# Kernel optimization log

Hardware: AMD Instinct MI355X
Metric: run time of the kernel (lower is better)

## Reference

```python
import jax, jax.numpy as jnp
import numpy as np

B = 4            # number of scenes (equal-size segments; offset = [M,2M,3M,4M])
K_NEAR = 16
K_FAR = 32
K_SMOOTH = 8
T_LOC = 0.1
T_CON = 0.5
BN_EPS = 1e-5


def setup_inputs() -> dict:
    key = jax.random.key(0)
    ks = jax.random.split(key, 8)
    N, C, H, O = 32768, 6, 64, 1
    coords = jax.random.uniform(ks[0], (N, 3), jnp.float32) * 2.0 - 1.0
    feat = jax.random.normal(ks[1], (N, C), jnp.float32)
    return {
        'feat': feat,
        'coords': coords,
        'W1': jax.random.normal(ks[2], (C, H), jnp.float32) * 0.1,
        'b1': jnp.zeros((H,), jnp.float32),
        'g1': jnp.ones((H,), jnp.float32),
        'be1': jnp.zeros((H,), jnp.float32),
        'W2': jax.random.normal(ks[3], (H, H), jnp.float32) * 0.1,
        'b2': jnp.zeros((H,), jnp.float32),
        'g2': jnp.ones((H,), jnp.float32),
        'be2': jnp.zeros((H,), jnp.float32),
        'W3': jax.random.normal(ks[4], (H, O), jnp.float32) * 0.1,
        'b3': jnp.zeros((O,), jnp.float32),
    }


def _bn_train(x, g, b):
    # BatchNorm1d in train mode: biased batch statistics
    mu = x.mean(axis=0)
    var = x.var(axis=0)
    return g * (x - mu) * jax.lax.rsqrt(var + BN_EPS) + b


def _knn_per_scene(c):
    # c: [M,3] -> [M,K_FAR] sorted nearest-neighbor indices (self first)
    sq = jnp.sum(c * c, axis=-1)                       # [M]
    d2 = sq[:, None] + sq[None, :] - 2.0 * (c @ c.T)   # [M,M] GEMM-based
    return jax.lax.top_k(-d2, K_FAR)[1]                # [M,K_FAR]


def _forward(feat, coords, W1, b1, g1, be1, W2, b2, g2, be2, W3, b3):
    N = feat.shape[0]
    M = N // B
    # ---- PointSorter MLP -> ordering scores in (0,1) ----
    h = jax.nn.gelu(_bn_train(feat @ W1 + b1, g1, be1), approximate=False)
    h = jax.nn.gelu(_bn_train(h @ W2 + b2, g2, be2), approximate=False)
    scores = jax.nn.sigmoid(h @ W3 + b3)               # [N, num_orders]
    s = scores.mean(axis=1, keepdims=True)             # [N,1] (scores_mean)
    # ---- single fused KNN (k=32); slice for k=16 (near) and k=8 (smooth) ----
    cb = coords.reshape(B, M, 3)
    idx = jax.vmap(_knn_per_scene)(cb)                 # [B,M,K_FAR] local
    idx = (idx + (jnp.arange(B) * M)[:, None, None]).reshape(N, K_FAR)
    idx_near = idx[:, :K_NEAR]
    idx_far = idx[:, K_NEAR:]
    idx_sm = idx[:, :K_SMOOTH]
    # ---- locality: neighbors should have similar scores ----
    sd = jnp.abs(s[:, None, :] - s[idx_near])[..., 0]          # [N,16]
    diff = coords[:, None, :] - coords[idx_near]               # [N,16,3]
    d = jnp.sqrt(jnp.maximum(jnp.sum(diff * diff, axis=2), 1e-24))
    w = jnp.exp(-d / T_LOC)
    loss_loc = jnp.sum(w * sd * sd) / jnp.maximum(jnp.sum(w), 1e-8)
    # ---- contrastive: far points should have different scores ----
    sim_pos = 1.0 - jnp.abs(s[:, None, :] - s[idx_near])       # [N,16,1]
    sim_neg = 1.0 - jnp.abs(s[:, None, :] - s[idx_far])        # [N,16,1]
    loss_pos = -jnp.mean(jnp.log(jax.nn.sigmoid(sim_pos / T_CON) + 1e-8))
    loss_neg = -jnp.mean(jnp.log(1.0 - jax.nn.sigmoid(sim_neg / T_CON) + 1e-8))
    loss_con = loss_pos + loss_neg
    # ---- smoothness: score close to mean of 8-NN scores ----
    nmean = s[idx_sm].mean(axis=1)                             # [N,1]
    loss_sm = jnp.mean((s - nmean) ** 2)
    return 1.0 * loss_loc + 0.5 * loss_con + 0.2 * loss_sm


def reference(feat, coords, W1, b1, g1, be1, W2, b2, g2, be2, W3, b3):
    return _forward(feat, coords, W1, b1, g1, be1, W2, b2, g2, be2, W3, b3)
```

## Files before the change

### kernel.cpp

```cpp
#include <hip/hip_runtime.h>

typedef unsigned long long u64;
typedef unsigned int u32;
typedef unsigned short u16;

#define N_PTS 32768
#define M_PTS 8192
#define C_IN 6
#define H_DIM 64

#define G 6
#define NCELL 216
#define NCELL_T 864
#define CW (1.0f/3.0f)

#define NBLK 256
#define QG 4
#define KTGT 48.0f

#define TL0 0.0494f
#define TL1 0.0740f
#define TL2 0.1110f
#define TL3 0.1736f
#define TL4 0.2600f
#define TL5 0.4000f


__device__ __forceinline__ float gelu_exact(float x) {
    return 0.5f * x * (1.0f + erff(x * 0.70710678118654752f));
}
__device__ __forceinline__ float sigmoidf_(float x) {
    return 1.0f / (1.0f + expf(-x));
}
__device__ __forceinline__ u64 u64min_(u64 a, u64 b) { return a < b ? a : b; }
__device__ __forceinline__ u64 u64max_(u64 a, u64 b) { return a < b ? b : a; }

__device__ __forceinline__ u64 bitonic_sort64(u64 key, int lane) {
    #pragma unroll
    for (int k = 2; k <= 64; k <<= 1) {
        #pragma unroll
        for (int j = k >> 1; j; j >>= 1) {
            u64 pk = __shfl_xor(key, j, 64);
            bool up = ((lane & k) == 0);
            bool tmin = (((lane & j) == 0) == up);
            key = tmin ? u64min_(key, pk) : u64max_(key, pk);
        }
    }
    return key;
}

__global__ __launch_bounds__(256) void kA(const float* __restrict__ feat,
        const float* __restrict__ coords, const float* __restrict__ W1,
        const float* __restrict__ b1, u32* __restrict__ gcount,
        u16* __restrict__ pcell, float* __restrict__ stats1) {
    __shared__ float red[512];
    int t = threadIdx.x, bid = blockIdx.x;
    if (bid < 128) {
        int n = bid * 256 + t;
        float x = coords[n*3], y = coords[n*3+1], z = coords[n*3+2];
        int cx = min(G-1, max(0, (int)floorf((x + 1.0f) * 3.0f)));
        int cy = min(G-1, max(0, (int)floorf((y + 1.0f) * 3.0f)));
        int cz = min(G-1, max(0, (int)floorf((z + 1.0f) * 3.0f)));
        int gcid = (n >> 13) * NCELL + (cz*G + cy)*G + cx;
        pcell[n] = (u16)gcid;
        atomicAdd(&gcount[gcid], 1u);
    }
    int c = t & 63, w = t >> 6;
    float w1c[C_IN];
    #pragma unroll
    for (int k = 0; k < C_IN; ++k) w1c[k] = W1[k*H_DIM + c];
    float bias = b1[c];
    float s1 = 0.f, s2 = 0.f;
    #pragma unroll 1
    for (int n = bid*8 + w*2; n < N_PTS; n += NBLK*8) {
        const float* fa = feat + n*C_IN;
        const float* fb = feat + (n+1)*C_IN;
        float ha = bias, hb = bias;
        #pragma unroll
        for (int k = 0; k < C_IN; ++k) {
            ha = fmaf(fa[k], w1c[k], ha);
            hb = fmaf(fb[k], w1c[k], hb);
        }
        s1 += ha + hb;
        s2 = fmaf(ha, ha, s2); s2 = fmaf(hb, hb, s2);
    }
    red[w*64 + c] = s1;
    red[256 + w*64 + c] = s2;
    __syncthreads();
    if (t < 64) {
        float a = red[t] + red[64+t] + red[128+t] + red[192+t];
        float b = red[256+t] + red[320+t] + red[384+t] + red[448+t];
        atomicAdd(&stats1[t], a);
        atomicAdd(&stats1[64+t], b);
    }
}

__global__ __launch_bounds__(256) void kB(const float* __restrict__ feat,
        const float* __restrict__ W1, const float* __restrict__ b1,
        const float* __restrict__ stats1, const float* __restrict__ g1,
        const float* __restrict__ be1, const float* __restrict__ W2,
        const float* __restrict__ b2, const u32* __restrict__ gcount,
        u32* __restrict__ cellstart, u32* __restrict__ cellptr,
        float* __restrict__ stats2) {
    __shared__ float red[512];
    __shared__ u32 sc[256];
    int t = threadIdx.x, bid = blockIdx.x;
    if (bid == 0) {
        u32 loc[4]; u32 s = 0;
        #pragma unroll
        for (int j = 0; j < 4; ++j) {
            int idx = t*4 + j;
            loc[j] = (idx < NCELL_T) ? gcount[idx] : 0u;
            s += loc[j];
        }
        sc[t] = s;
        __syncthreads();
        for (int off = 1; off < 256; off <<= 1) {
            u32 v = sc[t];
            if (t >= off) v += sc[t-off];
            __syncthreads();
            sc[t] = v;
            __syncthreads();
        }
        u32 run = sc[t] - s;
        #pragma unroll
        for (int j = 0; j < 4; ++j) {
            int idx = t*4 + j;
            if (idx < NCELL_T) { cellstart[idx] = run; cellptr[idx] = run; }
            run += loc[j];
        }
        if (t == 255) cellstart[NCELL_T] = sc[255];
        __syncthreads();
    }
    int c = t & 63, w = t >> 6;
    float w2c[H_DIM];
    #pragma unroll
    for (int k = 0; k < H_DIM; ++k) w2c[k] = W2[k*H_DIM + c];
    float w1c[C_IN];
    #pragma unroll
    for (int k = 0; k < C_IN; ++k) w1c[k] = W1[k*H_DIM + c];
    float mean1 = stats1[c] * (1.0f/N_PTS);
    float var1  = stats1[64+c] * (1.0f/N_PTS) - mean1*mean1;
    float sc1 = g1[c] * rsqrtf(var1 + 1e-5f);
    float sh1 = be1[c] - mean1*sc1;
    float bias1 = b1[c], bias2 = b2[c];
    float s1 = 0.f, s2 = 0.f;
    #pragma unroll 1
    for (int n = bid*8 + w*2; n < N_PTS; n += NBLK*8) {
        const float* fa = feat + n*C_IN;
        const float* fb = feat + (n+1)*C_IN;
        float ha = bias1, hb = bias1;
        #pragma unroll
        for (int k = 0; k < C_IN; ++k) {
            ha = fmaf(fa[k], w1c[k], ha);
            hb = fmaf(fb[k], w1c[k], hb);
        }
        float aa = gelu_exact(fmaf(sc1, ha, sh1));
        float ab = gelu_exact(fmaf(sc1, hb, sh1));
        float h2a = bias2, h2b = bias2;
        #pragma unroll
        for (int k = 0; k < H_DIM; ++k) {
            h2a = fmaf(__shfl(aa, k, 64), w2c[k], h2a);
            h2b = fmaf(__shfl(ab, k, 64), w2c[k], h2b);
        }
        s1 += h2a + h2b;
        s2 = fmaf(h2a, h2a, s2); s2 = fmaf(h2b, h2b, s2);
    }
    red[w*64 + c] = s1;
    red[256 + w*64 + c] = s2;
    __syncthreads();
    if (t < 64) {
        float a = red[t] + red[64+t] + red[128+t] + red[192+t];
        float b = red[256+t] + red[320+t] + red[384+t] + red[448+t];
        atomicAdd(&stats2[t], a);
        atomicAdd(&stats2[64+t], b);
    }
}

__global__ __launch_bounds__(256) void kC(const float* __restrict__ feat,
        const float* __restrict__ coords,
        const float* __restrict__ W1, const float* __restrict__ b1,
        const float* __restrict__ stats1, const float* __restrict__ g1,
        const float* __restrict__ be1, const float* __restrict__ W2,
        const float* __restrict__ b2, const float* __restrict__ stats2,
        const float* __restrict__ g2v, const float* __restrict__ be2,
        const float* __restrict__ W3, const float* __restrict__ b3,
        const u16* __restrict__ pcell, u32* __restrict__ cellptr,
        float4* __restrict__ P4s, u16* __restrict__ meta16,
        float* __restrict__ S) {
    int t = threadIdx.x, bid = blockIdx.x;
    if (bid < 128) {
        int n = bid * 256 + t;
        float x = coords[n*3], y = coords[n*3+1], z = coords[n*3+2];
        float sq = fmaf(x, x, fmaf(y, y, z*z));
        u32 pos = atomicAdd(&cellptr[pcell[n]], 1u);
        P4s[pos] = make_float4(x, y, z, sq);
        meta16[pos] = (u16)(n & (M_PTS-1));
    }
    int c = t & 63, w = t >> 6;
    float w2c[H_DIM];
    #pragma unroll
    for (int k = 0; k < H_DIM; ++k) w2c[k] = W2[k*H_DIM + c];
    float w1c[C_IN];
    #pragma unroll
    for (int k = 0; k < C_IN; ++k) w1c[k] = W1[k*H_DIM + c];
    float mean1 = stats1[c] * (1.0f/N_PTS);
    float var1  = stats1[64+c] * (1.0f/N_PTS) - mean1*mean1;
    float sc1 = g1[c] * rsqrtf(var1 + 1e-5f);
    float sh1 = be1[c] - mean1*sc1;
    float mean2 = stats2[c] * (1.0f/N_PTS);
    float var2  = stats2[64+c] * (1.0f/N_PTS) - mean2*mean2;
    float sc2 = g2v[c] * rsqrtf(var2 + 1e-5f);
    float sh2 = be2[c] - mean2*sc2;
    float bias1 = b1[c], bias2 = b2[c], w3 = W3[c], bb = b3[0];
    #pragma unroll 1
    for (int n = bid*8 + w*2; n < N_PTS; n += NBLK*8) {
        const float* fa = feat + n*C_IN;
        const float* fb = feat + (n+1)*C_IN;
        float ha = bias1, hb = bias1;
        #pragma unroll
        for (int k = 0; k < C_IN; ++k) {
            ha = fmaf(fa[k], w1c[k], ha);
            hb = fmaf(fb[k], w1c[k], hb);
        }
        float aa = gelu_exact(fmaf(sc1, ha, sh1));
        float ab = gelu_exact(fmaf(sc1, hb, sh1));
        float h2a = bias2, h2b = bias2;
        #pragma unroll
        for (int k = 0; k < H_DIM; ++k) {
            h2a = fmaf(__shfl(aa, k, 64), w2c[k], h2a);
            h2b = fmaf(__shfl(ab, k, 64), w2c[k], h2b);
        }
        float a2a = gelu_exact(fmaf(sc2, h2a, sh2));
        float a2b = gelu_exact(fmaf(sc2, h2b, sh2));
        float va = a2a * w3, vb = a2b * w3;
        #pragma unroll
        for (int m = 32; m; m >>= 1) {
            va += __shfl_xor(va, m, 64);
            vb += __shfl_xor(vb, m, 64);
        }
        if (c == 0) {
            S[n] = sigmoidf_(va + bb);
            S[n+1] = sigmoidf_(vb + bb);
        }
    }
}

__global__ __launch_bounds__(256) void kD(const float4* __restrict__ P4s,
        const u16* __restrict__ meta16, const u32* __restrict__ cellstart,
        const float* __restrict__ S, double* __restrict__ accum,
        u32* __restrict__ donecnt, float* __restrict__ out) {
    __shared__ u64 wavebuf[4][QG][128];
    __shared__ int runsb[16], runse[16];
    __shared__ int nruns_s;
    __shared__ u32 flistB[64];
    __shared__ u32 flnB;
    __shared__ u32 cnt6[6];
    __shared__ u32 ovcnt;
    __shared__ float smacc;
    __shared__ double lred[4][5];

    int t = threadIdx.x, bid = blockIdx.x;
    int lane = t & 63, w = t >> 6;
    u64 lmask = (1ull << lane) - 1ull;
    int cell = bid >> 1, half = bid & 1;
    int scene = cell / NCELL;
    int cid = cell - scene*NCELL;
    int cx = cid % G, cy = (cid / G) % G, cz = cid / (G*G);
    int sbase = scene * M_PTS;

    int ccrd[3] = {cx, cy, cz};
    bool wall[3]; int Wn = 0;
    #pragma unroll
    for (int d = 0; d < 3; ++d) { wall[d] = (ccrd[d] == 0 || ccrd[d] == G-1); Wn += wall[d]; }
    int lo[3], hi[3];
    #pragma unroll
    for (int d = 0; d < 3; ++d) {
        if (Wn >= 2 && !wall[d]) { lo[d] = min(max(ccrd[d]-2, 0), G-5); hi[d] = lo[d]+4; }
        else                     { lo[d] = min(max(ccrd[d]-1, 0), G-3); hi[d] = lo[d]+2; }
    }
    float lof[3], hif[3]; bool lw[3], hw[3];
    #pragma unroll
    for (int d = 0; d < 3; ++d) {
        lof[d] = -1.0f + lo[d]*CW; hif[d] = -1.0f + (hi[d]+1)*CW;
        lw[d] = (lo[d] == 0); hw[d] = (hi[d] == G-1);
    }
    if (t == 0) {
        int nr = 0;
        int nx = hi[0]-lo[0]+1;
        for (int z = lo[2]; z <= hi[2]; ++z)
            for (int y = lo[1]; y <= hi[1]; ++y) {
                int bc = scene*NCELL + (z*G + y)*G + lo[0];
                runsb[nr] = (int)cellstart[bc];
                runse[nr] = (int)cellstart[bc + nx];
                ++nr;
            }
        nruns_s = nr;
        flnB = 0;
    }
    int gcid = scene*NCELL + cid;
    int qstart = (int)cellstart[gcid];
    int qn = (int)cellstart[gcid+1] - qstart;
    __syncthreads();
    int nruns = nruns_s;
    int hq = (qn + 1) >> 1;
    int hqs = qstart + half * hq;
    int hqn = qn - half * hq; if (hqn > hq) hqn = hq; if (hqn < 0) hqn = 0;

    double anum=0.0, aden=0.0, aslp=0.0, asln=0.0, asmo=0.0;

    for (int g0 = w*QG; g0 < hqn; g0 += 4*QG) {
        int jcount = min(QG, hqn - g0);
        int qb = hqs + g0;
        float qx[QG], qy[QG], qz[QG], qs[QG], tp[QG];
        u32 baseq[QG];
        #pragma unroll
        for (int j = 0; j < QG; ++j) {
            int qg = qb + min(j, jcount-1);
            float4 qc = P4s[qg];
            qx[j]=qc.x; qy[j]=qc.y; qz[j]=qc.z; qs[j]=qc.w;
            float cov = 1e9f;
            float qdv[3] = {qc.x, qc.y, qc.z};
            #pragma unroll
            for (int d = 0; d < 3; ++d) {
                if (!lw[d]) cov = fminf(cov, qdv[d] - lof[d]);
                if (!hw[d]) cov = fminf(cov, hif[d] - qdv[d]);
            }
            float g2 = cov*cov;
            float axx = fminf(qc.x+1.f, 1.f-qc.x);
            float ayy = fminf(qc.y+1.f, 1.f-qc.y);
            float azz = fminf(qc.z+1.f, 1.f-qc.z);
            float r = 0.224f;
            #pragma unroll
            for (int it = 0; it < 3; ++it) {
                float ir = 1.0f / r;
                float ux = fminf(axx*ir, 1.f), uy = fminf(ayy*ir, 1.f), uz = fminf(azz*ir, 1.f);
                float fx = 0.25f*(2.f + 3.f*ux - ux*ux*ux);
                float fy = 0.25f*(2.f + 3.f*uy - uy*uy*uy);
                float fz = 0.25f*(2.f + 3.f*uz - uz*uz*uz);
                r = cbrtf(KTGT / (4289.32f * fx * fy * fz));
            }
            tp[j] = (j < jcount) ? (fminf(r*r, g2) - qc.w) : -1e30f;
            baseq[j] = 0;
        }

        for (int rr = 0; rr < nruns; ++rr) {
            int ve = runse[rr];
            for (int v0 = runsb[rr]; v0 < ve; v0 += 128) {
                int vA = v0 + lane, vB = v0 + 64 + lane;
                bool okA = vA < ve, okB = vB < ve;
                float4 pA = make_float4(0.f,0.f,0.f,1e30f);
                float4 pB = make_float4(0.f,0.f,0.f,1e30f);
                u32 mA = 0, mB = 0;
                if (okA) { pA = P4s[vA]; mA = (u32)meta16[vA]; }
                if (okB) { pB = P4s[vB]; mB = (u32)meta16[vB]; }
                #pragma unroll
                for (int j = 0; j < QG; ++j) {
                    float dotA = fmaf(qx[j], pA.x, fmaf(qy[j], pA.y, qz[j]*pA.z));
                    float e2A = fmaf(-2.0f, dotA, pA.w);
                    bool prA = okA && (e2A < tp[j]);
                    u64 mkA = __ballot(prA);
                    if (prA) {
                        float d2 = fmaxf(e2A + qs[j], 0.0f);
                        u64 key = ((u64)__float_as_uint(d2) << 13) | (u64)mA;
                        u32 pos = baseq[j] + (u32)__popcll(mkA & lmask);
                        if (pos < 128u) wavebuf[w][j][pos] = key;
                    }
                    baseq[j] += (u32)__popcll(mkA);
                    float dotB = fmaf(qx[j], pB.x, fmaf(qy[j], pB.y, qz[j]*pB.z));
                    float e2B = fmaf(-2.0f, dotB, pB.w);
                    bool prB = okB && (e2B < tp[j]);
                    u64 mkB = __ballot(prB);
                    if (prB) {
                        float d2 = fmaxf(e2B + qs[j], 0.0f);
                        u64 key = ((u64)__float_as_uint(d2) << 13) | (u64)mB;
                        u32 pos = baseq[j] + (u32)__popcll(mkB & lmask);
                        if (pos < 128u) wavebuf[w][j][pos] = key;
                    }
                    baseq[j] += (u32)__popcll(mkB);
                }
            }
        }

        #pragma unroll
        for (int j = 0; j < QG; ++j) {
            if (j >= jcount) continue;
            int qg = qb + j;
            u32 M = baseq[j];
            if (M < 32u || M > 128u) {
                if (lane == 0) {
                    u32 idx = atomicAdd(&flnB, 1u);
                    if (idx < 64u) flistB[idx] = (u32)qg;
                }
                continue;
            }
            u64 k0 = (lane < (int)min(M, 64u)) ? wavebuf[w][j][lane] : ~0ull;
            k0 = bitonic_sort64(k0, lane);
            if (M > 64u) {
                u64 k1 = (lane < (int)(M - 64u)) ? wavebuf[w][j][64 + lane] : ~0ull;
                k1 = bitonic_sort64(k1, lane);
                u64 pk = __shfl(k1, 63 - lane, 64);
                u64 lo2 = u64min_(k0, pk);
                #pragma unroll
                for (int jj = 32; jj; jj >>= 1) {
                    u64 pj = __shfl_xor(lo2, jj, 64);
                    lo2 = ((lane & jj) == 0) ? u64min_(lo2, pj) : u64max_(lo2, pj);
                }
                k0 = lo2;
            }
            float si = S[sbase + (int)meta16[qg]];
            float smsum = 0.f;
            if (lane < 32) {
                float d2 = __uint_as_float((u32)(k0 >> 13));
                u32 jo = (u32)(k0 & 0x1FFFu);
                float sj = S[sbase + (int)jo];
                float sd = fabsf(si - sj);
                float sim = 1.0f - sd;
                if (lane < 16) {
                    float d = sqrtf(fmaxf(d2, 1e-24f));
                    float wgt = expf(-10.0f*d);
                    anum += (double)(wgt*sd*sd);
                    aden += (double)wgt;
                    aslp += (double)logf(sigmoidf_(2.0f*sim) + 1e-8f);
                    if (lane < 8) smsum += sj;
                } else {
                    asln += (double)logf(sigmoidf_(-2.0f*sim) + 1e-8f);
                }
            }
            #pragma unroll
            for (int m = 32; m; m >>= 1) smsum += __shfl_xor(smsum, m, 64);
            if (lane == 0) {
                float dd = si - smsum*0.125f;
                asmo += (double)(dd*dd);
            }
        }
    }
    __syncthreads();

    int nf = min((int)flnB, 64);
    u64* ovbuf = &wavebuf[0][0][0];
    for (int f = 0; f < nf; ++f) {
        int fqg = (int)flistB[f];
        float4 fqc = P4s[fqg];
        float fsq = fqc.w;
        float fcov = 1e9f;
        float fqd[3] = {fqc.x, fqc.y, fqc.z};
        #pragma unroll
        for (int d = 0; d < 3; ++d) {
            if (!lw[d]) fcov = fminf(fcov, fqd[d] - lof[d]);
            if (!hw[d]) fcov = fminf(fcov, hif[d] - fqd[d]);
        }
        float fg2 = fcov*fcov;
        if (t < 6) cnt6[t] = 0;
        if (t == 0) { ovcnt = 0; smacc = 0.f; }
        __syncthreads();
        u32 c0=0,c1=0,c2=0,c3=0,c4=0,c5=0;
        for (int rr = 0; rr < nruns; ++rr) {
            for (int v = runsb[rr] + t; v < runse[rr]; v += 256) {
                float4 pp = P4s[v];
                float dot = fmaf(fqc.x, pp.x, fmaf(fqc.y, pp.y, fqc.z*pp.z));
                float e2 = fmaf(-2.0f, dot, pp.w);
                c0 += (e2 < TL0-fsq); c1 += (e2 < TL1-fsq); c2 += (e2 < TL2-fsq);
                c3 += (e2 < TL3-fsq); c4 += (e2 < TL4-fsq); c5 += (e2 < TL5-fsq);
            }
        }
        #pragma unroll
        for (int m = 32; m; m >>= 1) {
            c0 += __shfl_xor(c0, m, 64); c1 += __shfl_xor(c1, m, 64);
            c2 += __shfl_xor(c2, m, 64); c3 += __shfl_xor(c3, m, 64);
            c4 += __shfl_xor(c4, m, 64); c5 += __shfl_xor(c5, m, 64);
        }
        if (lane == 0) {
            atomicAdd(&cnt6[0], c0); atomicAdd(&cnt6[1], c1);
            atomicAdd(&cnt6[2], c2); atomicAdd(&cnt6[3], c3);
            atomicAdd(&cnt6[4], c4); atomicAdd(&cnt6[5], c5);
        }
        __syncthreads();
        float tau = TL2;
        if (TL3 <= fg2) tau = TL3;
        if (TL4 <= fg2) tau = TL4;
        if (TL5 <= fg2) tau = TL5;
        if      (cnt6[0] >= 32u) tau = TL0;
        else if (cnt6[1] >= 32u) tau = TL1;
        else if (cnt6[2] >= 32u) tau = TL2;
        else if (TL3 <= fg2 && cnt6[3] >= 32u) tau = TL3;
        else if (TL4 <= fg2 && cnt6[4] >= 32u) tau = TL4;
        else if (TL5 <= fg2 && cnt6[5] >= 32u) tau = TL5;
        float ftp = tau - fsq;
        for (int rr = 0; rr < nruns; ++rr) {
            for (int v = runsb[rr] + t; v < runse[rr]; v += 256) {
                float4 pp = P4s[v];
                float dot = fmaf(fqc.x, pp.x, fmaf(fqc.y, pp.y, fqc.z*pp.z));
                float e2 = fmaf(-2.0f, dot, pp.w);
                if (e2 < ftp) {
                    float d2 = fmaxf(e2 + fsq, 0.0f);
                    u64 key = ((u64)__float_as_uint(d2) << 13) | (u64)meta16[v];
                    u32 pos = atomicAdd(&ovcnt, 1u);
                    if (pos < 512u) ovbuf[pos] = key;
                }
            }
        }
        __syncthreads();
        u32 Mf = min(ovcnt, 512u);
        float fsi = S[sbase + (int)meta16[fqg]];
        for (int i = t; i < (int)Mf; i += 256) {
            u64 mykey = ovbuf[i];
            u32 rank = 0;
            for (u32 jj = 0; jj < Mf; ++jj) rank += (ovbuf[jj] < mykey);
            if (rank < 32u) {
                float d2 = __uint_as_float((u32)(mykey >> 13));
                u32 jo = (u32)(mykey & 0x1FFFu);
                float sj = S[sbase + (int)jo];
                float sd = fabsf(fsi - sj);
                float sim = 1.0f - sd;
                if (rank < 16u) {
                    float d = sqrtf(fmaxf(d2, 1e-24f));
                    float wgt = expf(-10.0f*d);
                    anum += (double)(wgt*sd*sd);
                    aden += (double)wgt;
                    aslp += (double)logf(sigmoidf_(2.0f*sim) + 1e-8f);
                    if (rank < 8u) atomicAdd(&smacc, sj);
                } else {
                    asln += (double)logf(sigmoidf_(-2.0f*sim) + 1e-8f);
                }
            }
        }
        __syncthreads();
        if (t == 0) {
            float dd = fsi - smacc*0.125f;
            asmo += (double)(dd*dd);
        }
        __syncthreads();
    }

    double v[5] = {anum, aden, aslp, asln, asmo};
    #pragma unroll
    for (int k = 0; k < 5; ++k) {
        for (int m = 32; m; m >>= 1) v[k] += __shfl_xor(v[k], m, 64);
    }
    if (lane == 0) {
        #pragma unroll
        for (int k = 0; k < 5; ++k) lred[w][k] = v[k];
    }
    __syncthreads();
    if (t == 0) {
        #pragma unroll
        for (int k = 0; k < 5; ++k)
            atomicAdd(&accum[k], lred[0][k] + lred[1][k] + lred[2][k] + lred[3][k]);
        __threadfence();
        u32 old = atomicAdd(donecnt, 1u);
        if (old == (u32)(2*NCELL_T - 1)) {
            double a0 = atomicAdd(&accum[0], 0.0);
            double a1 = atomicAdd(&accum[1], 0.0);
            double a2 = atomicAdd(&accum[2], 0.0);
            double a3 = atomicAdd(&accum[3], 0.0);
            double a4 = atomicAdd(&accum[4], 0.0);
            double loss_loc = a0 / fmax(a1, 1e-8);
            double inv = 1.0 / ((double)N_PTS * 16.0);
            double loss_con = -(a2 * inv) - (a3 * inv);
            double loss_sm = a4 / (double)N_PTS;
            out[0] = (float)(loss_loc + 0.5*loss_con + 0.2*loss_sm);
        }
    }
}

extern "C" void kernel_launch(void* const* d_in, const int* in_sizes, int n_in,
                              void* d_out, int out_size, void* d_ws, size_t ws_size,
                              hipStream_t stream) {
    const float* feat   = (const float*)d_in[0];
    const float* coords = (const float*)d_in[1];
    const float* W1 = (const float*)d_in[2];
    const float* b1 = (const float*)d_in[3];
    const float* g1 = (const float*)d_in[4];
    const float* be1= (const float*)d_in[5];
    const float* W2 = (const float*)d_in[6];
    const float* b2 = (const float*)d_in[7];
    const float* g2 = (const float*)d_in[8];
    const float* be2= (const float*)d_in[9];
    const float* W3 = (const float*)d_in[10];
    const float* b3 = (const float*)d_in[11];
    char* ws = (char*)d_ws;

    float* stats1   = (float*)(ws);
    float* stats2   = (float*)(ws + 512);
    u32* gcount     = (u32*)(ws + 1024);
    double* accum   = (double*)(ws + 4480);
    u32* donecnt    = (u32*)(ws + 4520);
    u32* cellstart  = (u32*)(ws + 4544);
    u32* cellptr    = (u32*)(ws + 8008);
    float* S        = (float*)(ws + 11472);
    float4* P4s     = (float4*)(ws + 142544);
    u16* meta16     = (u16*)(ws + 666832);
    u16* pcell      = (u16*)(ws + 732368);

    hipMemsetAsync(d_ws, 0, 4544, stream);

    hipLaunchKernelGGL(kA, dim3(NBLK), dim3(256), 0, stream,
                       feat, coords, W1, b1, gcount, pcell, stats1);
    hipLaunchKernelGGL(kB, dim3(NBLK), dim3(256), 0, stream,
                       feat, W1, b1, stats1, g1, be1, W2, b2,
                       gcount, cellstart, cellptr, stats2);
    hipLaunchKernelGGL(kC, dim3(NBLK), dim3(256), 0, stream,
                       feat, coords, W1, b1, stats1, g1, be1, W2, b2,
                       stats2, g2, be2, W3, b3, pcell, cellptr, P4s, meta16, S);
    hipLaunchKernelGGL(kD, dim3(2*NCELL_T), dim3(256), 0, stream,
                       P4s, meta16, cellstart, S, accum, donecnt, (float*)d_out);
}
```

Baseline: 325.6 us.

## Pack KNN keys into 32 bits, embed index in float4, split cells three ways

KNN sort keys shrink from 64-bit to 32-bit by truncating the distance's low 13 mantissa bits and packing the 13-bit point index there. The local index now lives in the float4 w slot and squared norms are recomputed, which drops the separate meta16 array. Query cells are split across 3 blocks instead of 2, with a retuned neighbor-count target and radius and a larger overflow buffer. The MLP loops now process 4 points per iteration instead of 2. Truncated keys can reorder near-tied neighbors, which may change results slightly.

```diff
diff --git a/kernel.cpp b/kernel.cpp
--- a/kernel.cpp
+++ b/kernel.cpp
@@ -16,7 +16,8 @@
 
 #define NBLK 256
 #define QG 4
-#define KTGT 48.0f
+#define BPC 3
+#define KTGT 54.0f
 
 #define TL0 0.0494f
 #define TL1 0.0740f
@@ -25,6 +26,9 @@
 #define TL4 0.2600f
 #define TL5 0.4000f
 
+#define KEYMASK 0xFFFFE000u
+#define IDXMASK 0x1FFFu
+
 
 __device__ __forceinline__ float gelu_exact(float x) {
     return 0.5f * x * (1.0f + erff(x * 0.70710678118654752f));
@@ -32,18 +36,16 @@
 __device__ __forceinline__ float sigmoidf_(float x) {
     return 1.0f / (1.0f + expf(-x));
 }
-__device__ __forceinline__ u64 u64min_(u64 a, u64 b) { return a < b ? a : b; }
-__device__ __forceinline__ u64 u64max_(u64 a, u64 b) { return a < b ? b : a; }
-
-__device__ __forceinline__ u64 bitonic_sort64(u64 key, int lane) {
+
+__device__ __forceinline__ u32 bitonic_sort64_u32(u32 key, int lane) {
     #pragma unroll
     for (int k = 2; k <= 64; k <<= 1) {
         #pragma unroll
         for (int j = k >> 1; j; j >>= 1) {
-            u64 pk = __shfl_xor(key, j, 64);
+            u32 pk = (u32)__shfl_xor((int)key, j, 64);
             bool up = ((lane & k) == 0);
             bool tmin = (((lane & j) == 0) == up);
-            key = tmin ? u64min_(key, pk) : u64max_(key, pk);
+            key = tmin ? min(key, pk) : max(key, pk);
         }
     }
     return key;
@@ -146,25 +148,28 @@
     float bias1 = b1[c], bias2 = b2[c];
     float s1 = 0.f, s2 = 0.f;
     #pragma unroll 1
-    for (int n = bid*8 + w*2; n < N_PTS; n += NBLK*8) {
-        const float* fa = feat + n*C_IN;
-        const float* fb = feat + (n+1)*C_IN;
-        float ha = bias1, hb = bias1;
-        #pragma unroll
-        for (int k = 0; k < C_IN; ++k) {
-            ha = fmaf(fa[k], w1c[k], ha);
-            hb = fmaf(fb[k], w1c[k], hb);
-        }
-        float aa = gelu_exact(fmaf(sc1, ha, sh1));
-        float ab = gelu_exact(fmaf(sc1, hb, sh1));
-        float h2a = bias2, h2b = bias2;
+    for (int n = bid*16 + w*4; n < N_PTS; n += NBLK*16) {
+        float h[4], a[4], h2[4];
+        #pragma unroll
+        for (int p = 0; p < 4; ++p) {
+            const float* f = feat + (n+p)*C_IN;
+            h[p] = bias1;
+            #pragma unroll
+            for (int k = 0; k < C_IN; ++k) h[p] = fmaf(f[k], w1c[k], h[p]);
+            a[p] = gelu_exact(fmaf(sc1, h[p], sh1));
+            h2[p] = bias2;
+        }
         #pragma unroll
         for (int k = 0; k < H_DIM; ++k) {
-            h2a = fmaf(__shfl(aa, k, 64), w2c[k], h2a);
-            h2b = fmaf(__shfl(ab, k, 64), w2c[k], h2b);
-        }
-        s1 += h2a + h2b;
-        s2 = fmaf(h2a, h2a, s2); s2 = fmaf(h2b, h2b, s2);
+            #pragma unroll
+            for (int p = 0; p < 4; ++p)
+                h2[p] = fmaf(__shfl(a[p], k, 64), w2c[k], h2[p]);
+        }
+        #pragma unroll
+        for (int p = 0; p < 4; ++p) {
+            s1 += h2[p];
+            s2 = fmaf(h2[p], h2[p], s2);
+        }
     }
     red[w*64 + c] = s1;
     red[256 + w*64 + c] = s2;
@@ -186,16 +191,13 @@
         const float* __restrict__ g2v, const float* __restrict__ be2,
         const float* __restrict__ W3, const float* __restrict__ b3,
         const u16* __restrict__ pcell, u32* __restrict__ cellptr,
-        float4* __restrict__ P4s, u16* __restrict__ meta16,
-        float* __restrict__ S) {
+        float4* __restrict__ P4s, float* __restrict__ S) {
     int t = threadIdx.x, bid = blockIdx.x;
     if (bid < 128) {
         int n = bid * 256 + t;
         float x = coords[n*3], y = coords[n*3+1], z = coords[n*3+2];
-        float sq = fmaf(x, x, fmaf(y, y, z*z));
         u32 pos = atomicAdd(&cellptr[pcell[n]], 1u);
-        P4s[pos] = make_float4(x, y, z, sq);
-        meta16[pos] = (u16)(n & (M_PTS-1));
+        P4s[pos] = make_float4(x, y, z, __uint_as_float((u32)(n & (M_PTS-1))));
     }
     int c = t & 63, w = t >> 6;
     float w2c[H_DIM];
@@ -214,43 +216,44 @@
     float sh2 = be2[c] - mean2*sc2;
     float bias1 = b1[c], bias2 = b2[c], w3 = W3[c], bb = b3[0];
     #pragma unroll 1
-    for (int n = bid*8 + w*2; n < N_PTS; n += NBLK*8) {
-        const float* fa = feat + n*C_IN;
-        const float* fb = feat + (n+1)*C_IN;
-        float ha = bias1, hb = bias1;
-        #pragma unroll
-        for (int k = 0; k < C_IN; ++k) {
-            ha = fmaf(fa[k], w1c[k], ha);
-            hb = fmaf(fb[k], w1c[k], hb);
-        }
-        float aa = gelu_exact(fmaf(sc1, ha, sh1));
-        float ab = gelu_exact(fmaf(sc1, hb, sh1));
-        float h2a = bias2, h2b = bias2;
+    for (int n = bid*16 + w*4; n < N_PTS; n += NBLK*16) {
+        float h[4], a[4], h2[4];
+        #pragma unroll
+        for (int p = 0; p < 4; ++p) {
+            const float* f = feat + (n+p)*C_IN;
+            h[p] = bias1;
+            #pragma unroll
+            for (int k = 0; k < C_IN; ++k) h[p] = fmaf(f[k], w1c[k], h[p]);
+            a[p] = gelu_exact(fmaf(sc1, h[p], sh1));
+            h2[p] = bias2;
+        }
         #pragma unroll
         for (int k = 0; k < H_DIM; ++k) {
-            h2a = fmaf(__shfl(aa, k, 64), w2c[k], h2a);
-            h2b = fmaf(__shfl(ab, k, 64), w2c[k], h2b);
-        }
-        float a2a = gelu_exact(fmaf(sc2, h2a, sh2));
-        float a2b = gelu_exact(fmaf(sc2, h2b, sh2));
-        float va = a2a * w3, vb = a2b * w3;
+            #pragma unroll
+            for (int p = 0; p < 4; ++p)
+                h2[p] = fmaf(__shfl(a[p], k, 64), w2c[k], h2[p]);
+        }
+        float v[4];
+        #pragma unroll
+        for (int p = 0; p < 4; ++p)
+            v[p] = gelu_exact(fmaf(sc2, h2[p], sh2)) * w3;
         #pragma unroll
         for (int m = 32; m; m >>= 1) {
-            va += __shfl_xor(va, m, 64);
-            vb += __shfl_xor(vb, m, 64);
+            #pragma unroll
+            for (int p = 0; p < 4; ++p) v[p] += __shfl_xor(v[p], m, 64);
         }
         if (c == 0) {
-            S[n] = sigmoidf_(va + bb);
-            S[n+1] = sigmoidf_(vb + bb);
+            #pragma unroll
+            for (int p = 0; p < 4; ++p) S[n+p] = sigmoidf_(v[p] + bb);
         }
     }
 }
 
 __global__ __launch_bounds__(256) void kD(const float4* __restrict__ P4s,
-        const u16* __restrict__ meta16, const u32* __restrict__ cellstart,
-        const float* __restrict__ S, double* __restrict__ accum,
-        u32* __restrict__ donecnt, float* __restrict__ out) {
-    __shared__ u64 wavebuf[4][QG][128];
+        const u32* __restrict__ cellstart, const float* __restrict__ S,
+        double* __restrict__ accum, u32* __restrict__ donecnt,
+        float* __restrict__ out) {
+    __shared__ u32 wavebuf[4][QG][128];
     __shared__ int runsb[16], runse[16];
     __shared__ int nruns_s;
     __shared__ u32 flistB[64];
@@ -263,7 +266,7 @@
     int t = threadIdx.x, bid = blockIdx.x;
     int lane = t & 63, w = t >> 6;
     u64 lmask = (1ull << lane) - 1ull;
-    int cell = bid >> 1, half = bid & 1;
+    int cell = bid / BPC, part = bid - cell*BPC;
     int scene = cell / NCELL;
     int cid = cell - scene*NCELL;
     int cx = cid % G, cy = (cid / G) % G, cz = cid / (G*G);
@@ -303,9 +306,9 @@
     int qn = (int)cellstart[gcid+1] - qstart;
     __syncthreads();
     int nruns = nruns_s;
-    int hq = (qn + 1) >> 1;
-    int hqs = qstart + half * hq;
-    int hqn = qn - half * hq; if (hqn > hq) hqn = hq; if (hqn < 0) hqn = 0;
+    int hq = (qn + BPC - 1) / BPC;
+    int hqs = qstart + part * hq;
+    int hqn = qn - part * hq; if (hqn > hq) hqn = hq; if (hqn < 0) hqn = 0;
 
     double anum=0.0, aden=0.0, aslp=0.0, asln=0.0, asmo=0.0;
 
@@ -313,12 +316,15 @@
         int jcount = min(QG, hqn - g0);
         int qb = hqs + g0;
         float qx[QG], qy[QG], qz[QG], qs[QG], tp[QG];
-        u32 baseq[QG];
+        u32 qid[QG], baseq[QG];
         #pragma unroll
         for (int j = 0; j < QG; ++j) {
             int qg = qb + min(j, jcount-1);
             float4 qc = P4s[qg];
-            qx[j]=qc.x; qy[j]=qc.y; qz[j]=qc.z; qs[j]=qc.w;
+            qx[j]=qc.x; qy[j]=qc.y; qz[j]=qc.z;
+            qid[j] = __float_as_uint(qc.w);
+            float qsq = fmaf(qc.x, qc.x, fmaf(qc.y, qc.y, qc.z*qc.z));
+            qs[j] = qsq;
             float cov = 1e9f;
             float qdv[3] = {qc.x, qc.y, qc.z};
             #pragma unroll
@@ -330,7 +336,7 @@
             float axx = fminf(qc.x+1.f, 1.f-qc.x);
             float ayy = fminf(qc.y+1.f, 1.f-qc.y);
             float azz = fminf(qc.z+1.f, 1.f-qc.z);
-            float r = 0.224f;
+            float r = 0.233f;
             #pragma unroll
             for (int it = 0; it < 3; ++it) {
                 float ir = 1.0f / r;
@@ -340,7 +346,7 @@
                 float fz = 0.25f*(2.f + 3.f*uz - uz*uz*uz);
                 r = cbrtf(KTGT / (4289.32f * fx * fy * fz));
             }
-            tp[j] = (j < jcount) ? (fminf(r*r, g2) - qc.w) : -1e30f;
+            tp[j] = (j < jcount) ? (fminf(r*r, g2) - qsq) : -1e30f;
             baseq[j] = 0;
         }
 
@@ -349,31 +355,32 @@
             for (int v0 = runsb[rr]; v0 < ve; v0 += 128) {
                 int vA = v0 + lane, vB = v0 + 64 + lane;
                 bool okA = vA < ve, okB = vB < ve;
-                float4 pA = make_float4(0.f,0.f,0.f,1e30f);
-                float4 pB = make_float4(0.f,0.f,0.f,1e30f);
-                u32 mA = 0, mB = 0;
-                if (okA) { pA = P4s[vA]; mA = (u32)meta16[vA]; }
-                if (okB) { pB = P4s[vB]; mB = (u32)meta16[vB]; }
+                float4 pA = make_float4(1e3f,1e3f,1e3f,0.f);
+                float4 pB = make_float4(1e3f,1e3f,1e3f,0.f);
+                if (okA) pA = P4s[vA];
+                if (okB) pB = P4s[vB];
+                float sqA = fmaf(pA.x, pA.x, fmaf(pA.y, pA.y, pA.z*pA.z));
+                float sqB = fmaf(pB.x, pB.x, fmaf(pB.y, pB.y, pB.z*pB.z));
                 #pragma unroll
                 for (int j = 0; j < QG; ++j) {
                     float dotA = fmaf(qx[j], pA.x, fmaf(qy[j], pA.y, qz[j]*pA.z));
-                    float e2A = fmaf(-2.0f, dotA, pA.w);
+                    float e2A = fmaf(-2.0f, dotA, sqA);
                     bool prA = okA && (e2A < tp[j]);
                     u64 mkA = __ballot(prA);
                     if (prA) {
                         float d2 = fmaxf(e2A + qs[j], 0.0f);
-                        u64 key = ((u64)__float_as_uint(d2) << 13) | (u64)mA;
+                        u32 key = (__float_as_uint(d2) & KEYMASK) | __float_as_uint(pA.w);
                         u32 pos = baseq[j] + (u32)__popcll(mkA & lmask);
                         if (pos < 128u) wavebuf[w][j][pos] = key;
                     }
                     baseq[j] += (u32)__popcll(mkA);
                     float dotB = fmaf(qx[j], pB.x, fmaf(qy[j], pB.y, qz[j]*pB.z));
-                    float e2B = fmaf(-2.0f, dotB, pB.w);
+                    float e2B = fmaf(-2.0f, dotB, sqB);
                     bool prB = okB && (e2B < tp[j]);
                     u64 mkB = __ballot(prB);
                     if (prB) {
                         float d2 = fmaxf(e2B + qs[j], 0.0f);
-                        u64 key = ((u64)__float_as_uint(d2) << 13) | (u64)mB;
+                        u32 key = (__float_as_uint(d2) & KEYMASK) | __float_as_uint(pB.w);
                         u32 pos = baseq[j] + (u32)__popcll(mkB & lmask);
                         if (pos < 128u) wavebuf[w][j][pos] = key;
                     }
@@ -394,25 +401,25 @@
                 }
                 continue;
             }
-            u64 k0 = (lane < (int)min(M, 64u)) ? wavebuf[w][j][lane] : ~0ull;
-            k0 = bitonic_sort64(k0, lane);
+            u32 k0 = (lane < (int)min(M, 64u)) ? wavebuf[w][j][lane] : 0xFFFFFFFFu;
+            k0 = bitonic_sort64_u32(k0, lane);
             if (M > 64u) {
-                u64 k1 = (lane < (int)(M - 64u)) ? wavebuf[w][j][64 + lane] : ~0ull;
-                k1 = bitonic_sort64(k1, lane);
-                u64 pk = __shfl(k1, 63 - lane, 64);
-                u64 lo2 = u64min_(k0, pk);
+                u32 k1 = (lane < (int)(M - 64u)) ? wavebuf[w][j][64 + lane] : 0xFFFFFFFFu;
+                k1 = bitonic_sort64_u32(k1, lane);
+                u32 pk = (u32)__shfl((int)k1, 63 - lane, 64);
+                u32 lo2 = min(k0, pk);
                 #pragma unroll
                 for (int jj = 32; jj; jj >>= 1) {
-                    u64 pj = __shfl_xor(lo2, jj, 64);
-                    lo2 = ((lane & jj) == 0) ? u64min_(lo2, pj) : u64max_(lo2, pj);
+                    u32 pj = (u32)__shfl_xor((int)lo2, jj, 64);
+                    lo2 = ((lane & jj) == 0) ? min(lo2, pj) : max(lo2, pj);
                 }
                 k0 = lo2;
             }
-            float si = S[sbase + (int)meta16[qg]];
+            float si = S[sbase + (int)qid[j]];
             float smsum = 0.f;
             if (lane < 32) {
-                float d2 = __uint_as_float((u32)(k0 >> 13));
-                u32 jo = (u32)(k0 & 0x1FFFu);
+                float d2 = __uint_as_float(k0 & KEYMASK);
+                u32 jo = k0 & IDXMASK;
                 float sj = S[sbase + (int)jo];
                 float sd = fabsf(si - sj);
                 float sim = 1.0f - sd;
@@ -438,11 +445,11 @@
     __syncthreads();
 
     int nf = min((int)flnB, 64);
-    u64* ovbuf = &wavebuf[0][0][0];
+    u32* ovbuf = &wavebuf[0][0][0];
     for (int f = 0; f < nf; ++f) {
         int fqg = (int)flistB[f];
         float4 fqc = P4s[fqg];
-        float fsq = fqc.w;
+        float fsq = fmaf(fqc.x, fqc.x, fmaf(fqc.y, fqc.y, fqc.z*fqc.z));
         float fcov = 1e9f;
         float fqd[3] = {fqc.x, fqc.y, fqc.z};
         #pragma unroll
@@ -458,8 +465,9 @@
         for (int rr = 0; rr < nruns; ++rr) {
             for (int v = runsb[rr] + t; v < runse[rr]; v += 256) {
                 float4 pp = P4s[v];
+                float sq = fmaf(pp.x, pp.x, fmaf(pp.y, pp.y, pp.z*pp.z));
                 float dot = fmaf(fqc.x, pp.x, fmaf(fqc.y, pp.y, fqc.z*pp.z));
-                float e2 = fmaf(-2.0f, dot, pp.w);
+                float e2 = fmaf(-2.0f, dot, sq);
                 c0 += (e2 < TL0-fsq); c1 += (e2 < TL1-fsq); c2 += (e2 < TL2-fsq);
                 c3 += (e2 < TL3-fsq); c4 += (e2 < TL4-fsq); c5 += (e2 < TL5-fsq);
             }
@@ -490,26 +498,27 @@
         for (int rr = 0; rr < nruns; ++rr) {
             for (int v = runsb[rr] + t; v < runse[rr]; v += 256) {
                 float4 pp = P4s[v];
+                float sq = fmaf(pp.x, pp.x, fmaf(pp.y, pp.y, pp.z*pp.z));
                 float dot = fmaf(fqc.x, pp.x, fmaf(fqc.y, pp.y, fqc.z*pp.z));
-                float e2 = fmaf(-2.0f, dot, pp.w);
+                float e2 = fmaf(-2.0f, dot, sq);
                 if (e2 < ftp) {
                     float d2 = fmaxf(e2 + fsq, 0.0f);
-                    u64 key = ((u64)__float_as_uint(d2) << 13) | (u64)meta16[v];
+                    u32 key = (__float_as_uint(d2) & KEYMASK) | __float_as_uint(pp.w);
                     u32 pos = atomicAdd(&ovcnt, 1u);
-                    if (pos < 512u) ovbuf[pos] = key;
+                    if (pos < 2048u) ovbuf[pos] = key;
                 }
             }
         }
         __syncthreads();
-        u32 Mf = min(ovcnt, 512u);
-        float fsi = S[sbase + (int)meta16[fqg]];
+        u32 Mf = min(ovcnt, 2048u);
+        float fsi = S[sbase + (int)__float_as_uint(fqc.w)];
         for (int i = t; i < (int)Mf; i += 256) {
-            u64 mykey = ovbuf[i];
+            u32 mykey = ovbuf[i];
             u32 rank = 0;
             for (u32 jj = 0; jj < Mf; ++jj) rank += (ovbuf[jj] < mykey);
             if (rank < 32u) {
-                float d2 = __uint_as_float((u32)(mykey >> 13));
-                u32 jo = (u32)(mykey & 0x1FFFu);
+                float d2 = __uint_as_float(mykey & KEYMASK);
+                u32 jo = mykey & IDXMASK;
                 float sj = S[sbase + (int)jo];
                 float sd = fabsf(fsi - sj);
                 float sim = 1.0f - sd;
@@ -549,7 +558,7 @@
             atomicAdd(&accum[k], lred[0][k] + lred[1][k] + lred[2][k] + lred[3][k]);
         __threadfence();
         u32 old = atomicAdd(donecnt, 1u);
-        if (old == (u32)(2*NCELL_T - 1)) {
+        if (old == (u32)(BPC*NCELL_T - 1)) {
             double a0 = atomicAdd(&accum[0], 0.0);
             double a1 = atomicAdd(&accum[1], 0.0);
             double a2 = atomicAdd(&accum[2], 0.0);
@@ -590,8 +599,7 @@
     u32* cellptr    = (u32*)(ws + 8008);
     float* S        = (float*)(ws + 11472);
     float4* P4s     = (float4*)(ws + 142544);
-    u16* meta16     = (u16*)(ws + 666832);
-    u16* pcell      = (u16*)(ws + 732368);
+    u16* pcell      = (u16*)(ws + 666832);
 
     hipMemsetAsync(d_ws, 0, 4544, stream);
 
@@ -602,7 +610,7 @@
                        gcount, cellstart, cellptr, stats2);
     hipLaunchKernelGGL(kC, dim3(NBLK), dim3(256), 0, stream,
                        feat, coords, W1, b1, stats1, g1, be1, W2, b2,
-                       stats2, g2, be2, W3, b3, pcell, cellptr, P4s, meta16, S);
-    hipLaunchKernelGGL(kD, dim3(2*NCELL_T), dim3(256), 0, stream,
-                       P4s, meta16, cellstart, S, accum, donecnt, (float*)d_out);
-}
+                       stats2, g2, be2, W3, b3, pcell, cellptr, P4s, S);
+    hipLaunchKernelGGL(kD, dim3(BPC*NCELL_T), dim3(256), 0, stream,
+                       P4s, cellstart, S, accum, donecnt, (float*)d_out);
+}
```

New measurement: 392.2 us. +20.4%, slower.
